# Kernel tuning notes

Measured on AMD Instinct MI355X. Metric: run time of the kernel, lower is better.

## Reference

```python
import jax, jax.numpy as jnp
import numpy as np

D_MODEL = 1024
N_HEAD = 16
D_K = D_MODEL // N_HEAD


def setup_inputs() -> dict:
    key = jax.random.key(0)
    ks = jax.random.split(key, 7)
    B, S = 4, 2048
    scale = 1.0 / np.sqrt(D_MODEL)
    x = jax.random.normal(ks[0], (B, S, D_MODEL), dtype=jnp.float32)
    Wq = jax.random.normal(ks[1], (D_MODEL, D_MODEL), dtype=jnp.float32) * scale
    Wk = jax.random.normal(ks[2], (D_MODEL, D_MODEL), dtype=jnp.float32) * scale
    Wv = jax.random.normal(ks[3], (D_MODEL, D_MODEL), dtype=jnp.float32) * scale
    bq = jax.random.normal(ks[4], (D_MODEL,), dtype=jnp.float32) * 0.01
    bk = jax.random.normal(ks[5], (D_MODEL,), dtype=jnp.float32) * 0.01
    bv = jax.random.normal(ks[6], (D_MODEL,), dtype=jnp.float32) * 0.01
    return {"x": x, "Wq": Wq, "bq": bq, "Wk": Wk, "bk": bk, "Wv": Wv, "bv": bv}


def reference(x, Wq, bq, Wk, bk, Wv, bv):
    B, S, _ = x.shape
    # QKV projections (nn.Linear: x @ W.T + b; weights here stored as [in, out])
    Q = x @ Wq + bq  # [B, S, D]
    K = x @ Wk + bk
    V = x @ Wv + bv
    # split heads -> [B, H, S, d_k]
    def split(t):
        return t.reshape(B, S, N_HEAD, D_K).transpose(0, 2, 1, 3)
    Qh, Kh, Vh = split(Q), split(K), split(V)
    scores = jnp.einsum('bhqd,bhkd->bhqk', Qh, Kh) / jnp.sqrt(jnp.float32(D_K))
    attn = jax.nn.softmax(scores, axis=-1)
    ctx = jnp.einsum('bhqk,bhkd->bhqd', attn, Vh)  # [B, H, S, d_k]
    return ctx.transpose(0, 2, 1, 3).reshape(B, S, D_MODEL)
```

## Files before the change

### kernel.cpp

```cpp
#include <hip/hip_runtime.h>
#include <stdint.h>

#define D_MODEL 1024
#define NHEAD   16
#define DK      64
#define BATCH   4
#define SEQ     2048
#define MTOT    (BATCH*SEQ)
#define KVB     64
#define NT      (SEQ/KVB)

typedef __attribute__((ext_vector_type(4)))  float  f32x4;
typedef __attribute__((ext_vector_type(16))) float  f32x16;
typedef __attribute__((ext_vector_type(8)))  __bf16 bf16x8;
typedef __attribute__((ext_vector_type(8)))  unsigned short u16x8;
typedef __attribute__((ext_vector_type(4)))  unsigned int u32x4;

#define QSCALE 0.1803368801111244f

__device__ __forceinline__ unsigned short f2bf(float f) {
    unsigned u = __builtin_bit_cast(unsigned, f);
    u += 0x7fffu + ((u >> 16) & 1u);
    return (unsigned short)(u >> 16);
}

__global__ __launch_bounds__(256) void cvt_fused_kernel(const float* __restrict__ x,
                                                        const float* __restrict__ Wq,
                                                        const float* __restrict__ Wk,
                                                        const float* __restrict__ Wv,
                                                        unsigned short* __restrict__ xb,
                                                        unsigned short* __restrict__ wt) {
    __shared__ float tile[32][33];
    int bid = blockIdx.x;
    int tid = threadIdx.x;
    if (bid < 4096) {
        size_t i = ((size_t)bid * 256 + tid) * 8;
        f32x4 a = *(const f32x4*)(x + i);
        f32x4 b = *(const f32x4*)(x + i + 4);
        u16x8 o;
        o[0] = f2bf(a[0]); o[1] = f2bf(a[1]); o[2] = f2bf(a[2]); o[3] = f2bf(a[3]);
        o[4] = f2bf(b[0]); o[5] = f2bf(b[1]); o[6] = f2bf(b[2]); o[7] = f2bf(b[3]);
        *(u16x8*)(xb + i) = o;
        return;
    }
    int wid = bid - 4096;
    int mat = wid >> 10;
    int r   = wid & 1023;
    int n0  = (r & 31) * 32;
    int k0  = (r >> 5) * 32;
    int tx  = tid & 31;
    int ty  = tid >> 5;
    const float* W = (mat == 0) ? Wq : (mat == 1) ? Wk : Wv;
    #pragma unroll
    for (int i = 0; i < 4; ++i)
        tile[ty + i*8][tx] = W[(size_t)(k0 + ty + i*8) * D_MODEL + n0 + tx];
    __syncthreads();
    unsigned short* dst = wt + (size_t)mat * D_MODEL * D_MODEL;
    #pragma unroll
    for (int i = 0; i < 4; ++i)
        dst[(size_t)(n0 + ty + i*8) * D_MODEL + k0 + tx] = f2bf(tile[tx][ty + i*8]);
}

#define BM 128
#define BN 128
#define BKK 64
__global__ __launch_bounds__(256) void qkv_gemm_kernel(const unsigned short* __restrict__ xb,
                                                       const unsigned short* __restrict__ wt,
                                                       const float* __restrict__ bq,
                                                       const float* __restrict__ bk,
                                                       const float* __restrict__ bv,
                                                       unsigned short* __restrict__ qkv) {
    __shared__ __align__(16) unsigned char sA[BM * BKK * 2];
    __shared__ __align__(16) unsigned char sB[BN * BKK * 2];

    int lin = blockIdx.y * 24 + blockIdx.x;
    lin = (lin & 7) * 192 + (lin >> 3);
    int nb   = lin % 24;
    int mb   = lin / 24;
    int mat  = nb >> 3;
    int col0 = (nb & 7) * BN;
    int m0   = mb * BM;
    int t    = threadIdx.x;
    int lane = t & 63;
    int w    = t >> 6;

    const unsigned short* wmat = wt + (size_t)mat * D_MODEL * D_MODEL;
    const float* bias = (mat == 0) ? bq : (mat == 1) ? bk : bv;

    f32x4 acc[4][4];
    #pragma unroll
    for (int i = 0; i < 4; ++i)
        #pragma unroll
        for (int j = 0; j < 4; ++j)
            acc[i][j] = (f32x4)0.0f;

    int rA = (w >> 1) * 64;
    int rB = (w & 1) * 64;

    for (int ks = 0; ks < D_MODEL / BKK; ++ks) {
        int K0 = ks * BKK;
        #pragma unroll
        for (int i = 0; i < 4; ++i) {
            int c   = t + 256 * i;
            int row = c >> 3;
            int kc  = c & 7;
            int swz = kc ^ (row & 7);
            const unsigned short* ga = xb + (size_t)(m0 + row) * D_MODEL + K0 + swz * 8;
            __builtin_amdgcn_global_load_lds(
                (const __attribute__((address_space(1))) void*)ga,
                (__attribute__((address_space(3))) void*)(sA + c * 16), 16, 0, 0);
            const unsigned short* gb = wmat + (size_t)(col0 + row) * D_MODEL + K0 + swz * 8;
            __builtin_amdgcn_global_load_lds(
                (const __attribute__((address_space(1))) void*)gb,
                (__attribute__((address_space(3))) void*)(sB + c * 16), 16, 0, 0);
        }
        __syncthreads();

        #pragma unroll
        for (int kk = 0; kk < 2; ++kk) {
            bf16x8 af[4], bf[4];
            int kc = kk * 4 + (lane >> 4);
            #pragma unroll
            for (int mt = 0; mt < 4; ++mt) {
                int row = rA + mt * 16 + (lane & 15);
                int swz = kc ^ (row & 7);
                af[mt] = *(const bf16x8*)(sA + row * 128 + swz * 16);
            }
            #pragma unroll
            for (int nt = 0; nt < 4; ++nt) {
                int row = rB + nt * 16 + (lane & 15);
                int swz = kc ^ (row & 7);
                bf[nt] = *(const bf16x8*)(sB + row * 128 + swz * 16);
            }
            #pragma unroll
            for (int mt = 0; mt < 4; ++mt)
                #pragma unroll
                for (int nt = 0; nt < 4; ++nt)
                    acc[mt][nt] = __builtin_amdgcn_mfma_f32_16x16x32_bf16(
                        af[mt], bf[nt], acc[mt][nt], 0, 0, 0);
        }
        __syncthreads();
    }

    #pragma unroll
    for (int mt = 0; mt < 4; ++mt) {
        #pragma unroll
        for (int nt = 0; nt < 4; ++nt) {
            int gn = col0 + rB + nt * 16 + (lane & 15);
            float bval = bias[gn];
            #pragma unroll
            for (int r = 0; r < 4; ++r) {
                int gm = m0 + rA + mt * 16 + (lane >> 4) * 4 + r;
                float v = acc[mt][nt][r] + bval;
                if (mat == 0) v *= QSCALE;
                int b = gm >> 11, s = gm & 2047;
                int h = gn >> 6,  d = gn & 63;
                size_t idx;
                if (mat == 2)
                    idx = ((size_t)(b * NHEAD + h) * DK + d) * SEQ + s;
                else
                    idx = ((size_t)(b * NHEAD + h) * SEQ + s) * DK + d;
                qkv[(size_t)mat * MTOT * D_MODEL + idx] = f2bf(v);
            }
        }
    }
}

#define CVTPK(dst, lo_, hi_) \
    asm("v_cvt_pk_bf16_f32 %0, %1, %2" : "=v"(dst) : "v"(lo_), "v"(hi_))
#define PLSWAP(x_, y_) \
    asm("v_permlane32_swap_b32 %0, %1" : "+v"(x_), "+v"(y_))
#define EXP2(dst, x_) \
    asm("v_exp_f32 %0, %1" : "=v"(dst) : "v"(x_))

__device__ __forceinline__ bf16x8 make_pf(float p0, float p1, float p2, float p3,
                                          float p4, float p5, float p6, float p7) {
    unsigned a1, a2, b1, b2;
    CVTPK(a1, p0, p1); CVTPK(a2, p2, p3);
    CVTPK(b1, p4, p5); CVTPK(b2, p6, p7);
    PLSWAP(a1, b1); PLSWAP(a2, b2);
    u32x4 u = { a1, a2, b1, b2 };
    return __builtin_bit_cast(bf16x8, u);
}

__device__ __forceinline__ float vmax16(const f32x16& v) {
    float a = fmaxf(fmaxf(v[0],  v[1]),  v[2]);
    float b = fmaxf(fmaxf(v[3],  v[4]),  v[5]);
    float c = fmaxf(fmaxf(v[6],  v[7]),  v[8]);
    float d = fmaxf(fmaxf(v[9],  v[10]), v[11]);
    a = fmaxf(fmaxf(a, v[12]), v[13]);
    b = fmaxf(fmaxf(b, v[14]), v[15]);
    return fmaxf(fmaxf(a, b), fmaxf(c, d));
}

__global__ __launch_bounds__(512, 2) void attn_kernel(const unsigned short* __restrict__ qkv,
                                                      float* __restrict__ out) {
    __shared__ __align__(16) unsigned char lds[49152];

    int bh = blockIdx.x;
    int qb = blockIdx.y;
    int t = threadIdx.x;
    int lane = t & 63;
    int w = t >> 6;
    int hi = lane >> 5;
    int l31 = lane & 31;

    const unsigned short* Qb = qkv + (size_t)bh * SEQ * DK;
    const unsigned short* Kb = qkv + (size_t)MTOT * D_MODEL + (size_t)bh * SEQ * DK;
    const unsigned short* Vt = qkv + (size_t)2 * MTOT * D_MODEL + (size_t)bh * DK * SEQ;

    int qbase = qb * 256 + w * 32;

    bf16x8 aq[4];
    #pragma unroll
    for (int kd = 0; kd < 4; ++kd)
        aq[kd] = *(const bf16x8*)(Qb + (size_t)(qbase + l31) * DK + kd * 16 + hi * 8);

    f32x16 o0 = (f32x16)0.0f, o1 = (f32x16)0.0f;
    float mrun = -3e38f, lrun = 0.0f;

#define STAGE(tile_, b_) do {                                                          \
    int kv0_ = (tile_) * KVB;                                                          \
    int row_ = t >> 3, kc_ = t & 7;                                                    \
    int sw_ = (kc_ ^ (row_ & 7)) * 8;                                                  \
    __builtin_amdgcn_global_load_lds(                                                  \
        (const __attribute__((address_space(1))) void*)(Kb + (size_t)(kv0_ + row_) * DK + sw_), \
        (__attribute__((address_space(3))) void*)(lds + (b_) * 8192 + t * 16), 16, 0, 0);       \
    __builtin_amdgcn_global_load_lds(                                                  \
        (const __attribute__((address_space(1))) void*)(Vt + (size_t)row_ * SEQ + kv0_ + sw_),  \
        (__attribute__((address_space(3))) void*)(lds + 24576 + (b_) * 8192 + t * 16), 16, 0, 0); \
} while (0)

    int swz7 = l31 & 7;
    int cofs0 = ((0 + hi) ^ swz7) << 4;
    int cofs1 = ((2 + hi) ^ swz7) << 4;
    int cofs2 = ((4 + hi) ^ swz7) << 4;
    int cofs3 = ((6 + hi) ^ swz7) << 4;

    STAGE(0, 0);
    STAGE(1, 1);
    asm volatile("s_waitcnt vmcnt(2)" ::: "memory");
    __builtin_amdgcn_s_barrier();

    int b0 = 0, b1 = 1, b2 = 2;

    for (int kt = 0; kt < NT; ++kt) {
        if (kt + 2 < NT)
            STAGE(kt + 2, b2);

        const unsigned char* kb = lds + b0 * 8192;
        const unsigned char* vb = lds + 24576 + b0 * 8192;
        const unsigned char* kr0 = kb + l31 * 128;
        const unsigned char* kr1 = kb + (32 + l31) * 128;
        const unsigned char* vr0 = vb + l31 * 128;
        const unsigned char* vr1 = vb + (32 + l31) * 128;

        bf16x8 ak00 = *(const bf16x8*)(kr0 + cofs0);
        bf16x8 ak01 = *(const bf16x8*)(kr0 + cofs1);
        bf16x8 ak02 = *(const bf16x8*)(kr0 + cofs2);
        bf16x8 ak03 = *(const bf16x8*)(kr0 + cofs3);
        bf16x8 ak10 = *(const bf16x8*)(kr1 + cofs0);
        bf16x8 ak11 = *(const bf16x8*)(kr1 + cofs1);
        bf16x8 ak12 = *(const bf16x8*)(kr1 + cofs2);
        bf16x8 ak13 = *(const bf16x8*)(kr1 + cofs3);
        f32x16 sc0 = (f32x16)0.0f, sc1 = (f32x16)0.0f;
        __builtin_amdgcn_s_setprio(1);
        sc0 = __builtin_amdgcn_mfma_f32_32x32x16_bf16(ak00, aq[0], sc0, 0, 0, 0);
        sc1 = __builtin_amdgcn_mfma_f32_32x32x16_bf16(ak10, aq[0], sc1, 0, 0, 0);
        sc0 = __builtin_amdgcn_mfma_f32_32x32x16_bf16(ak01, aq[1], sc0, 0, 0, 0);
        sc1 = __builtin_amdgcn_mfma_f32_32x32x16_bf16(ak11, aq[1], sc1, 0, 0, 0);
        sc0 = __builtin_amdgcn_mfma_f32_32x32x16_bf16(ak02, aq[2], sc0, 0, 0, 0);
        sc1 = __builtin_amdgcn_mfma_f32_32x32x16_bf16(ak12, aq[2], sc1, 0, 0, 0);
        sc0 = __builtin_amdgcn_mfma_f32_32x32x16_bf16(ak03, aq[3], sc0, 0, 0, 0);
        sc1 = __builtin_amdgcn_mfma_f32_32x32x16_bf16(ak13, aq[3], sc1, 0, 0, 0);
        __builtin_amdgcn_s_setprio(0);

        bf16x8 av00 = *(const bf16x8*)(vr0 + cofs0);
        bf16x8 av01 = *(const bf16x8*)(vr0 + cofs1);
        bf16x8 av02 = *(const bf16x8*)(vr0 + cofs2);
        bf16x8 av03 = *(const bf16x8*)(vr0 + cofs3);
        bf16x8 av10 = *(const bf16x8*)(vr1 + cofs0);
        bf16x8 av11 = *(const bf16x8*)(vr1 + cofs1);
        bf16x8 av12 = *(const bf16x8*)(vr1 + cofs2);
        bf16x8 av13 = *(const bf16x8*)(vr1 + cofs3);

        float mx = fmaxf(vmax16(sc0), vmax16(sc1));
        mx = fmaxf(mx, __shfl_xor(mx, 32));
        if (!__all(mx <= mrun + 8.0f)) {
            float mnew = fmaxf(mrun, mx);
            float al;  EXP2(al, mrun - mnew);
            lrun *= al;
            #pragma unroll
            for (int i = 0; i < 16; ++i) { o0[i] *= al; o1[i] *= al; }
            mrun = mnew;
        }
        #pragma unroll
        for (int i = 0; i < 16; ++i) { float p; EXP2(p, sc0[i] - mrun); sc0[i] = p; }
        #pragma unroll
        for (int i = 0; i < 16; ++i) { float p; EXP2(p, sc1[i] - mrun); sc1[i] = p; }
        float r0 = 0.f, r1 = 0.f, r2 = 0.f, r3 = 0.f;
        #pragma unroll
        for (int i = 0; i < 4; ++i) {
            r0 += sc0[i] + sc1[i];     r1 += sc0[4+i] + sc1[4+i];
            r2 += sc0[8+i] + sc1[8+i]; r3 += sc0[12+i] + sc1[12+i];
        }
        float rs = (r0 + r1) + (r2 + r3);
        rs += __shfl_xor(rs, 32);
        lrun += rs;

        bf16x8 pf0 = make_pf(sc0[0], sc0[1], sc0[2],  sc0[3],  sc0[4],  sc0[5],  sc0[6],  sc0[7]);
        bf16x8 pf1 = make_pf(sc0[8], sc0[9], sc0[10], sc0[11], sc0[12], sc0[13], sc0[14], sc0[15]);
        bf16x8 pf2 = make_pf(sc1[0], sc1[1], sc1[2],  sc1[3],  sc1[4],  sc1[5],  sc1[6],  sc1[7]);
        bf16x8 pf3 = make_pf(sc1[8], sc1[9], sc1[10], sc1[11], sc1[12], sc1[13], sc1[14], sc1[15]);

        __builtin_amdgcn_s_setprio(1);
        o0 = __builtin_amdgcn_mfma_f32_32x32x16_bf16(av00, pf0, o0, 0, 0, 0);
        o1 = __builtin_amdgcn_mfma_f32_32x32x16_bf16(av10, pf0, o1, 0, 0, 0);
        o0 = __builtin_amdgcn_mfma_f32_32x32x16_bf16(av01, pf1, o0, 0, 0, 0);
        o1 = __builtin_amdgcn_mfma_f32_32x32x16_bf16(av11, pf1, o1, 0, 0, 0);
        o0 = __builtin_amdgcn_mfma_f32_32x32x16_bf16(av02, pf2, o0, 0, 0, 0);
        o1 = __builtin_amdgcn_mfma_f32_32x32x16_bf16(av12, pf2, o1, 0, 0, 0);
        o0 = __builtin_amdgcn_mfma_f32_32x32x16_bf16(av03, pf3, o0, 0, 0, 0);
        o1 = __builtin_amdgcn_mfma_f32_32x32x16_bf16(av13, pf3, o1, 0, 0, 0);
        __builtin_amdgcn_s_setprio(0);

        if (kt + 2 < NT) {
            asm volatile("s_waitcnt vmcnt(2)" ::: "memory");
            __builtin_amdgcn_s_barrier();
        } else if (kt + 1 < NT) {
            asm volatile("s_waitcnt vmcnt(0)" ::: "memory");
            __builtin_amdgcn_s_barrier();
        }
        int tb = b0; b0 = b1; b1 = b2; b2 = tb;
    }
#undef STAGE

    int b = bh >> 4, h = bh & 15;
    float rl = 1.0f / lrun;
    float* dst = out + ((size_t)b * SEQ + qbase + l31) * D_MODEL + h * DK;
    #pragma unroll
    for (int g = 0; g < 4; ++g) {
        int d0 = 8 * g + 4 * hi;
        f32x4 v0 = { o0[4*g] * rl, o0[4*g+1] * rl, o0[4*g+2] * rl, o0[4*g+3] * rl };
        *(f32x4*)(dst + d0) = v0;
        f32x4 v1 = { o1[4*g] * rl, o1[4*g+1] * rl, o1[4*g+2] * rl, o1[4*g+3] * rl };
        *(f32x4*)(dst + 32 + d0) = v1;
    }
}

extern "C" void kernel_launch(void* const* d_in, const int* in_sizes, int n_in,
                              void* d_out, int out_size, void* d_ws, size_t ws_size,
                              hipStream_t stream) {
    const float* x  = (const float*)d_in[0];
    const float* Wq = (const float*)d_in[1];
    const float* bq = (const float*)d_in[2];
    const float* Wk = (const float*)d_in[3];
    const float* bk = (const float*)d_in[4];
    const float* Wv = (const float*)d_in[5];
    const float* bv = (const float*)d_in[6];
    float* out = (float*)d_out;

    unsigned short* xb  = (unsigned short*)d_ws;
    unsigned short* wt  = xb + (size_t)MTOT * D_MODEL;
    unsigned short* qkv = wt + (size_t)3 * D_MODEL * D_MODEL;

    cvt_fused_kernel<<<dim3(7168), dim3(256), 0, stream>>>(x, Wq, Wk, Wv, xb, wt);
    qkv_gemm_kernel<<<dim3(24, 64), dim3(256), 0, stream>>>(xb, wt, bq, bk, bv, qkv);
    attn_kernel<<<dim3(64, 8), dim3(512), 0, stream>>>(qkv, out);
}
```

Before: 196.5 us.

## Process two 32-row Q tiles per wave in attention, halving wave count

Each wave now handles 64 query rows as two 32-row tiles (A and B), so every K/V fragment read from LDS is reused for twice as many MFMAs. The block shrinks from 512 to 256 threads, and each thread issues two async global-to-LDS loads per operand per stage, with the vmcnt waits adjusted to match. The aim is to cut LDS read traffic per FLOP and raise MFMA density. The cost is roughly double the accumulator and score registers per wave, which could lower occupancy or cause spills, and fewer waves are available to hide latency.

```diff
diff --git a/kernel.cpp b/kernel.cpp
--- a/kernel.cpp
+++ b/kernel.cpp
@@ -193,7 +193,7 @@
     return fmaxf(fmaxf(a, b), fmaxf(c, d));
 }
 
-__global__ __launch_bounds__(512, 2) void attn_kernel(const unsigned short* __restrict__ qkv,
+__global__ __launch_bounds__(256, 2) void attn_kernel(const unsigned short* __restrict__ qkv,
                                                       float* __restrict__ out) {
     __shared__ __align__(16) unsigned char lds[49152];
 
@@ -209,26 +209,35 @@
     const unsigned short* Kb = qkv + (size_t)MTOT * D_MODEL + (size_t)bh * SEQ * DK;
     const unsigned short* Vt = qkv + (size_t)2 * MTOT * D_MODEL + (size_t)bh * DK * SEQ;
 
-    int qbase = qb * 256 + w * 32;
-
-    bf16x8 aq[4];
+    int qbase0 = qb * 256 + w * 64;
+    int qbase1 = qbase0 + 32;
+
+    bf16x8 aqA[4], aqB[4];
     #pragma unroll
-    for (int kd = 0; kd < 4; ++kd)
-        aq[kd] = *(const bf16x8*)(Qb + (size_t)(qbase + l31) * DK + kd * 16 + hi * 8);
-
-    f32x16 o0 = (f32x16)0.0f, o1 = (f32x16)0.0f;
-    float mrun = -3e38f, lrun = 0.0f;
+    for (int kd = 0; kd < 4; ++kd) {
+        aqA[kd] = *(const bf16x8*)(Qb + (size_t)(qbase0 + l31) * DK + kd * 16 + hi * 8);
+        aqB[kd] = *(const bf16x8*)(Qb + (size_t)(qbase1 + l31) * DK + kd * 16 + hi * 8);
+    }
+
+    f32x16 oA0 = (f32x16)0.0f, oA1 = (f32x16)0.0f;
+    f32x16 oB0 = (f32x16)0.0f, oB1 = (f32x16)0.0f;
+    float mrunA = -3e38f, lrunA = 0.0f;
+    float mrunB = -3e38f, lrunB = 0.0f;
 
 #define STAGE(tile_, b_) do {                                                          \
     int kv0_ = (tile_) * KVB;                                                          \
-    int row_ = t >> 3, kc_ = t & 7;                                                    \
-    int sw_ = (kc_ ^ (row_ & 7)) * 8;                                                  \
-    __builtin_amdgcn_global_load_lds(                                                  \
-        (const __attribute__((address_space(1))) void*)(Kb + (size_t)(kv0_ + row_) * DK + sw_), \
-        (__attribute__((address_space(3))) void*)(lds + (b_) * 8192 + t * 16), 16, 0, 0);       \
-    __builtin_amdgcn_global_load_lds(                                                  \
-        (const __attribute__((address_space(1))) void*)(Vt + (size_t)row_ * SEQ + kv0_ + sw_),  \
-        (__attribute__((address_space(3))) void*)(lds + 24576 + (b_) * 8192 + t * 16), 16, 0, 0); \
+    _Pragma("unroll")                                                                  \
+    for (int i_ = 0; i_ < 2; ++i_) {                                                   \
+        int c_ = t + 256 * i_;                                                         \
+        int row_ = c_ >> 3, kc_ = c_ & 7;                                              \
+        int sw_ = (kc_ ^ (row_ & 7)) * 8;                                              \
+        __builtin_amdgcn_global_load_lds(                                              \
+            (const __attribute__((address_space(1))) void*)(Kb + (size_t)(kv0_ + row_) * DK + sw_), \
+            (__attribute__((address_space(3))) void*)(lds + (b_) * 8192 + c_ * 16), 16, 0, 0);      \
+        __builtin_amdgcn_global_load_lds(                                              \
+            (const __attribute__((address_space(1))) void*)(Vt + (size_t)row_ * SEQ + kv0_ + sw_),  \
+            (__attribute__((address_space(3))) void*)(lds + 24576 + (b_) * 8192 + c_ * 16), 16, 0, 0); \
+    }                                                                                  \
 } while (0)
 
     int swz7 = l31 & 7;
@@ -239,7 +248,7 @@
 
     STAGE(0, 0);
     STAGE(1, 1);
-    asm volatile("s_waitcnt vmcnt(2)" ::: "memory");
+    asm volatile("s_waitcnt vmcnt(4)" ::: "memory");
     __builtin_amdgcn_s_barrier();
 
     int b0 = 0, b1 = 1, b2 = 2;
@@ -263,16 +272,26 @@
         bf16x8 ak11 = *(const bf16x8*)(kr1 + cofs1);
         bf16x8 ak12 = *(const bf16x8*)(kr1 + cofs2);
         bf16x8 ak13 = *(const bf16x8*)(kr1 + cofs3);
-        f32x16 sc0 = (f32x16)0.0f, sc1 = (f32x16)0.0f;
+
+        f32x16 scA0 = (f32x16)0.0f, scA1 = (f32x16)0.0f;
+        f32x16 scB0 = (f32x16)0.0f, scB1 = (f32x16)0.0f;
         __builtin_amdgcn_s_setprio(1);
-        sc0 = __builtin_amdgcn_mfma_f32_32x32x16_bf16(ak00, aq[0], sc0, 0, 0, 0);
-        sc1 = __builtin_amdgcn_mfma_f32_32x32x16_bf16(ak10, aq[0], sc1, 0, 0, 0);
-        sc0 = __builtin_amdgcn_mfma_f32_32x32x16_bf16(ak01, aq[1], sc0, 0, 0, 0);
-        sc1 = __builtin_amdgcn_mfma_f32_32x32x16_bf16(ak11, aq[1], sc1, 0, 0, 0);
-        sc0 = __builtin_amdgcn_mfma_f32_32x32x16_bf16(ak02, aq[2], sc0, 0, 0, 0);
-        sc1 = __builtin_amdgcn_mfma_f32_32x32x16_bf16(ak12, aq[2], sc1, 0, 0, 0);
-        sc0 = __builtin_amdgcn_mfma_f32_32x32x16_bf16(ak03, aq[3], sc0, 0, 0, 0);
-        sc1 = __builtin_amdgcn_mfma_f32_32x32x16_bf16(ak13, aq[3], sc1, 0, 0, 0);
+        scA0 = __builtin_amdgcn_mfma_f32_32x32x16_bf16(ak00, aqA[0], scA0, 0, 0, 0);
+        scA1 = __builtin_amdgcn_mfma_f32_32x32x16_bf16(ak10, aqA[0], scA1, 0, 0, 0);
+        scB0 = __builtin_amdgcn_mfma_f32_32x32x16_bf16(ak00, aqB[0], scB0, 0, 0, 0);
+        scB1 = __builtin_amdgcn_mfma_f32_32x32x16_bf16(ak10, aqB[0], scB1, 0, 0, 0);
+        scA0 = __builtin_amdgcn_mfma_f32_32x32x16_bf16(ak01, aqA[1], scA0, 0, 0, 0);
+        scA1 = __builtin_amdgcn_mfma_f32_32x32x16_bf16(ak11, aqA[1], scA1, 0, 0, 0);
+        scB0 = __builtin_amdgcn_mfma_f32_32x32x16_bf16(ak01, aqB[1], scB0, 0, 0, 0);
+        scB1 = __builtin_amdgcn_mfma_f32_32x32x16_bf16(ak11, aqB[1], scB1, 0, 0, 0);
+        scA0 = __builtin_amdgcn_mfma_f32_32x32x16_bf16(ak02, aqA[2], scA0, 0, 0, 0);
+        scA1 = __builtin_amdgcn_mfma_f32_32x32x16_bf16(ak12, aqA[2], scA1, 0, 0, 0);
+        scB0 = __builtin_amdgcn_mfma_f32_32x32x16_bf16(ak02, aqB[2], scB0, 0, 0, 0);
+        scB1 = __builtin_amdgcn_mfma_f32_32x32x16_bf16(ak12, aqB[2], scB1, 0, 0, 0);
+        scA0 = __builtin_amdgcn_mfma_f32_32x32x16_bf16(ak03, aqA[3], scA0, 0, 0, 0);
+        scA1 = __builtin_amdgcn_mfma_f32_32x32x16_bf16(ak13, aqA[3], scA1, 0, 0, 0);
+        scB0 = __builtin_amdgcn_mfma_f32_32x32x16_bf16(ak03, aqB[3], scB0, 0, 0, 0);
+        scB1 = __builtin_amdgcn_mfma_f32_32x32x16_bf16(ak13, aqB[3], scB1, 0, 0, 0);
         __builtin_amdgcn_s_setprio(0);
 
         bf16x8 av00 = *(const bf16x8*)(vr0 + cofs0);
@@ -284,48 +303,92 @@
         bf16x8 av12 = *(const bf16x8*)(vr1 + cofs2);
         bf16x8 av13 = *(const bf16x8*)(vr1 + cofs3);
 
-        float mx = fmaxf(vmax16(sc0), vmax16(sc1));
-        mx = fmaxf(mx, __shfl_xor(mx, 32));
-        if (!__all(mx <= mrun + 8.0f)) {
-            float mnew = fmaxf(mrun, mx);
-            float al;  EXP2(al, mrun - mnew);
-            lrun *= al;
-            #pragma unroll
-            for (int i = 0; i < 16; ++i) { o0[i] *= al; o1[i] *= al; }
-            mrun = mnew;
-        }
-        #pragma unroll
-        for (int i = 0; i < 16; ++i) { float p; EXP2(p, sc0[i] - mrun); sc0[i] = p; }
-        #pragma unroll
-        for (int i = 0; i < 16; ++i) { float p; EXP2(p, sc1[i] - mrun); sc1[i] = p; }
-        float r0 = 0.f, r1 = 0.f, r2 = 0.f, r3 = 0.f;
-        #pragma unroll
-        for (int i = 0; i < 4; ++i) {
-            r0 += sc0[i] + sc1[i];     r1 += sc0[4+i] + sc1[4+i];
-            r2 += sc0[8+i] + sc1[8+i]; r3 += sc0[12+i] + sc1[12+i];
-        }
-        float rs = (r0 + r1) + (r2 + r3);
-        rs += __shfl_xor(rs, 32);
-        lrun += rs;
-
-        bf16x8 pf0 = make_pf(sc0[0], sc0[1], sc0[2],  sc0[3],  sc0[4],  sc0[5],  sc0[6],  sc0[7]);
-        bf16x8 pf1 = make_pf(sc0[8], sc0[9], sc0[10], sc0[11], sc0[12], sc0[13], sc0[14], sc0[15]);
-        bf16x8 pf2 = make_pf(sc1[0], sc1[1], sc1[2],  sc1[3],  sc1[4],  sc1[5],  sc1[6],  sc1[7]);
-        bf16x8 pf3 = make_pf(sc1[8], sc1[9], sc1[10], sc1[11], sc1[12], sc1[13], sc1[14], sc1[15]);
-
-        __builtin_amdgcn_s_setprio(1);
-        o0 = __builtin_amdgcn_mfma_f32_32x32x16_bf16(av00, pf0, o0, 0, 0, 0);
-        o1 = __builtin_amdgcn_mfma_f32_32x32x16_bf16(av10, pf0, o1, 0, 0, 0);
-        o0 = __builtin_amdgcn_mfma_f32_32x32x16_bf16(av01, pf1, o0, 0, 0, 0);
-        o1 = __builtin_amdgcn_mfma_f32_32x32x16_bf16(av11, pf1, o1, 0, 0, 0);
-        o0 = __builtin_amdgcn_mfma_f32_32x32x16_bf16(av02, pf2, o0, 0, 0, 0);
-        o1 = __builtin_amdgcn_mfma_f32_32x32x16_bf16(av12, pf2, o1, 0, 0, 0);
-        o0 = __builtin_amdgcn_mfma_f32_32x32x16_bf16(av03, pf3, o0, 0, 0, 0);
-        o1 = __builtin_amdgcn_mfma_f32_32x32x16_bf16(av13, pf3, o1, 0, 0, 0);
-        __builtin_amdgcn_s_setprio(0);
+        {
+            float mx = fmaxf(vmax16(scA0), vmax16(scA1));
+            mx = fmaxf(mx, __shfl_xor(mx, 32));
+            if (!__all(mx <= mrunA + 8.0f)) {
+                float mnew = fmaxf(mrunA, mx);
+                float al;  EXP2(al, mrunA - mnew);
+                lrunA *= al;
+                #pragma unroll
+                for (int i = 0; i < 16; ++i) { oA0[i] *= al; oA1[i] *= al; }
+                mrunA = mnew;
+            }
+            #pragma unroll
+            for (int i = 0; i < 16; ++i) { float p; EXP2(p, scA0[i] - mrunA); scA0[i] = p; }
+            #pragma unroll
+            for (int i = 0; i < 16; ++i) { float p; EXP2(p, scA1[i] - mrunA); scA1[i] = p; }
+            float r0 = 0.f, r1 = 0.f, r2 = 0.f, r3 = 0.f;
+            #pragma unroll
+            for (int i = 0; i < 4; ++i) {
+                r0 += scA0[i] + scA1[i];     r1 += scA0[4+i] + scA1[4+i];
+                r2 += scA0[8+i] + scA1[8+i]; r3 += scA0[12+i] + scA1[12+i];
+            }
+            float rs = (r0 + r1) + (r2 + r3);
+            rs += __shfl_xor(rs, 32);
+            lrunA += rs;
+
+            bf16x8 pf0 = make_pf(scA0[0], scA0[1], scA0[2],  scA0[3],  scA0[4],  scA0[5],  scA0[6],  scA0[7]);
+            bf16x8 pf1 = make_pf(scA0[8], scA0[9], scA0[10], scA0[11], scA0[12], scA0[13], scA0[14], scA0[15]);
+            bf16x8 pf2 = make_pf(scA1[0], scA1[1], scA1[2],  scA1[3],  scA1[4],  scA1[5],  scA1[6],  scA1[7]);
+            bf16x8 pf3 = make_pf(scA1[8], scA1[9], scA1[10], scA1[11], scA1[12], scA1[13], scA1[14], scA1[15]);
+
+            __builtin_amdgcn_s_setprio(1);
+            oA0 = __builtin_amdgcn_mfma_f32_32x32x16_bf16(av00, pf0, oA0, 0, 0, 0);
+            oA1 = __builtin_amdgcn_mfma_f32_32x32x16_bf16(av10, pf0, oA1, 0, 0, 0);
+            oA0 = __builtin_amdgcn_mfma_f32_32x32x16_bf16(av01, pf1, oA0, 0, 0, 0);
+            oA1 = __builtin_amdgcn_mfma_f32_32x32x16_bf16(av11, pf1, oA1, 0, 0, 0);
+            oA0 = __builtin_amdgcn_mfma_f32_32x32x16_bf16(av02, pf2, oA0, 0, 0, 0);
+            oA1 = __builtin_amdgcn_mfma_f32_32x32x16_bf16(av12, pf2, oA1, 0, 0, 0);
+            oA0 = __builtin_amdgcn_mfma_f32_32x32x16_bf16(av03, pf3, oA0, 0, 0, 0);
+            oA1 = __builtin_amdgcn_mfma_f32_32x32x16_bf16(av13, pf3, oA1, 0, 0, 0);
+            __builtin_amdgcn_s_setprio(0);
+        }
+
+        {
+            float mx = fmaxf(vmax16(scB0), vmax16(scB1));
+            mx = fmaxf(mx, __shfl_xor(mx, 32));
+            if (!__all(mx <= mrunB + 8.0f)) {
+                float mnew = fmaxf(mrunB, mx);
+                float al;  EXP2(al, mrunB - mnew);
+                lrunB *= al;
+                #pragma unroll
+                for (int i = 0; i < 16; ++i) { oB0[i] *= al; oB1[i] *= al; }
+                mrunB = mnew;
+            }
+            #pragma unroll
+            for (int i = 0; i < 16; ++i) { float p; EXP2(p, scB0[i] - mrunB); scB0[i] = p; }
+            #pragma unroll
+            for (int i = 0; i < 16; ++i) { float p; EXP2(p, scB1[i] - mrunB); scB1[i] = p; }
+            float r0 = 0.f, r1 = 0.f, r2 = 0.f, r3 = 0.f;
+            #pragma unroll
+            for (int i = 0; i < 4; ++i) {
+                r0 += scB0[i] + scB1[i];     r1 += scB0[4+i] + scB1[4+i];
+                r2 += scB0[8+i] + scB1[8+i]; r3 += scB0[12+i] + scB1[12+i];
+            }
+            float rs = (r0 + r1) + (r2 + r3);
+            rs += __shfl_xor(rs, 32);
+            lrunB += rs;
+
+            bf16x8 pf0 = make_pf(scB0[0], scB0[1], scB0[2],  scB0[3],  scB0[4],  scB0[5],  scB0[6],  scB0[7]);
+            bf16x8 pf1 = make_pf(scB0[8], scB0[9], scB0[10], scB0[11], scB0[12], scB0[13], scB0[14], scB0[15]);
+            bf16x8 pf2 = make_pf(scB1[0], scB1[1], scB1[2],  scB1[3],  scB1[4],  scB1[5],  scB1[6],  scB1[7]);
+            bf16x8 pf3 = make_pf(scB1[8], scB1[9], scB1[10], scB1[11], scB1[12], scB1[13], scB1[14], scB1[15]);
+
+            __builtin_amdgcn_s_setprio(1);
+            oB0 = __builtin_amdgcn_mfma_f32_32x32x16_bf16(av00, pf0, oB0, 0, 0, 0);
+            oB1 = __builtin_amdgcn_mfma_f32_32x32x16_bf16(av10, pf0, oB1, 0, 0, 0);
+            oB0 = __builtin_amdgcn_mfma_f32_32x32x16_bf16(av01, pf1, oB0, 0, 0, 0);
+            oB1 = __builtin_amdgcn_mfma_f32_32x32x16_bf16(av11, pf1, oB1, 0, 0, 0);
+            oB0 = __builtin_amdgcn_mfma_f32_32x32x16_bf16(av02, pf2, oB0, 0, 0, 0);
+            oB1 = __builtin_amdgcn_mfma_f32_32x32x16_bf16(av12, pf2, oB1, 0, 0, 0);
+            oB0 = __builtin_amdgcn_mfma_f32_32x32x16_bf16(av03, pf3, oB0, 0, 0, 0);
+            oB1 = __builtin_amdgcn_mfma_f32_32x32x16_bf16(av13, pf3, oB1, 0, 0, 0);
+            __builtin_amdgcn_s_setprio(0);
+        }
 
         if (kt + 2 < NT) {
-            asm volatile("s_waitcnt vmcnt(2)" ::: "memory");
+            asm volatile("s_waitcnt vmcnt(4)" ::: "memory");
             __builtin_amdgcn_s_barrier();
         } else if (kt + 1 < NT) {
             asm volatile("s_waitcnt vmcnt(0)" ::: "memory");
@@ -336,15 +399,29 @@
 #undef STAGE
 
     int b = bh >> 4, h = bh & 15;
-    float rl = 1.0f / lrun;
-    float* dst = out + ((size_t)b * SEQ + qbase + l31) * D_MODEL + h * DK;
-    #pragma unroll
-    for (int g = 0; g < 4; ++g) {
-        int d0 = 8 * g + 4 * hi;
-        f32x4 v0 = { o0[4*g] * rl, o0[4*g+1] * rl, o0[4*g+2] * rl, o0[4*g+3] * rl };
-        *(f32x4*)(dst + d0) = v0;
-        f32x4 v1 = { o1[4*g] * rl, o1[4*g+1] * rl, o1[4*g+2] * rl, o1[4*g+3] * rl };
-        *(f32x4*)(dst + 32 + d0) = v1;
+    {
+        float rl = 1.0f / lrunA;
+        float* dst = out + ((size_t)b * SEQ + qbase0 + l31) * D_MODEL + h * DK;
+        #pragma unroll
+        for (int g = 0; g < 4; ++g) {
+            int d0 = 8 * g + 4 * hi;
+            f32x4 v0 = { oA0[4*g] * rl, oA0[4*g+1] * rl, oA0[4*g+2] * rl, oA0[4*g+3] * rl };
+            *(f32x4*)(dst + d0) = v0;
+            f32x4 v1 = { oA1[4*g] * rl, oA1[4*g+1] * rl, oA1[4*g+2] * rl, oA1[4*g+3] * rl };
+            *(f32x4*)(dst + 32 + d0) = v1;
+        }
+    }
+    {
+        float rl = 1.0f / lrunB;
+        float* dst = out + ((size_t)b * SEQ + qbase1 + l31) * D_MODEL + h * DK;
+        #pragma unroll
+        for (int g = 0; g < 4; ++g) {
+            int d0 = 8 * g + 4 * hi;
+            f32x4 v0 = { oB0[4*g] * rl, oB0[4*g+1] * rl, oB0[4*g+2] * rl, oB0[4*g+3] * rl };
+            *(f32x4*)(dst + d0) = v0;
+            f32x4 v1 = { oB1[4*g] * rl, oB1[4*g+1] * rl, oB1[4*g+2] * rl, oB1[4*g+3] * rl };
+            *(f32x4*)(dst + 32 + d0) = v1;
+        }
     }
 }
 
@@ -366,5 +443,5 @@
 
     cvt_fused_kernel<<<dim3(7168), dim3(256), 0, stream>>>(x, Wq, Wk, Wv, xb, wt);
     qkv_gemm_kernel<<<dim3(24, 64), dim3(256), 0, stream>>>(xb, wt, bq, bk, bv, qkv);
-    attn_kernel<<<dim3(64, 8), dim3(512), 0, stream>>>(qkv, out);
-}
+    attn_kernel<<<dim3(64, 8), dim3(256), 0, stream>>>(qkv, out);
+}
```

New measurement: 188.8 us. -3.9%, faster.
